# Performance work log

Measured on AMD Instinct MI355X. Metric: run time of the kernel, lower is better.

The kernel has to match this reference:

```python
import jax, jax.numpy as jnp
import numpy as np

B, IN_DIM, HV_DIM, NUM_CLASSES = 16384, 2048, 8192, 1000


def setup_inputs() -> dict:
    key = jax.random.key(0)
    kx, kp, kc = jax.random.split(key, 3)
    x = jax.random.normal(kx, (B, IN_DIM), dtype=jnp.float32)
    # +/-1 random projection and class hypervectors (2*bernoulli - 1), as in the torch buffers
    proj = (jax.random.randint(kp, (IN_DIM, HV_DIM), 0, 2) * 2 - 1).astype(jnp.float32)
    class_hv = (jax.random.randint(kc, (HV_DIM, NUM_CLASSES), 0, 2) * 2 - 1).astype(jnp.float32)
    return {"x": x, "proj": proj, "class_hv": class_hv}


def reference(x, proj, class_hv):
    # dense projection -> sign binarize -> binary associative-memory matmul (score_mode='dot')
    hv = x @ proj                                   # [B, HV_DIM]
    hv_bin = jnp.where(hv >= 0, 1.0, -1.0).astype(hv.dtype)
    scores = hv_bin @ class_hv                      # [B, NUM_CLASSES]
    return scores, hv_bin
```

## Files before the change

### kernel.cpp

```cpp
#include <hip/hip_runtime.h>
#include <hip/hip_bf16.h>

typedef _Float16 half8  __attribute__((ext_vector_type(8)));
typedef _Float16 half4_t __attribute__((ext_vector_type(4)));
typedef float    floatx4 __attribute__((ext_vector_type(4)));
typedef int      intx4   __attribute__((ext_vector_type(4)));

#define B_DIM   16384
#define IN_D    2048
#define HV_D    8192
#define NC      1000
#define NCP     1024
#define SCORES_N (B_DIM * NC)

#define GLD16(gp, lp) __builtin_amdgcn_global_load_lds( \
    (const __attribute__((address_space(1))) void*)(gp), \
    (__attribute__((address_space(3))) void*)(lp), 16, 0, 0)

__global__ void k_split(const float* __restrict__ x, _Float16* __restrict__ xh,
                        _Float16* __restrict__ xl) {
    size_t i = (size_t)blockIdx.x * 256 + threadIdx.x;
    floatx4 v = ((const floatx4*)x)[i];
    half4_t h, l;
#pragma unroll
    for (int j = 0; j < 4; ++j) {
        _Float16 hh = (_Float16)v[j];
        h[j] = hh;
        l[j] = (_Float16)(v[j] - (float)hh);
    }
    ((half4_t*)xh)[i] = h;
    ((half4_t*)xl)[i] = l;
}

__global__ void k_transpose_proj(const float* __restrict__ p, _Float16* __restrict__ pT) {
    __shared__ float tile[64][65];
    const int t = threadIdx.x;
    const int nt = blockIdx.x * 64;
    const int kt = blockIdx.y * 64;
    const int tr = t >> 4, tc = (t & 15) * 4;
#pragma unroll
    for (int s = 0; s < 4; ++s) {
        int r = tr + s * 16;
        floatx4 v = *(const floatx4*)&p[(size_t)(kt + r) * HV_D + nt + tc];
        tile[r][tc] = v[0]; tile[r][tc + 1] = v[1];
        tile[r][tc + 2] = v[2]; tile[r][tc + 3] = v[3];
    }
    __syncthreads();
#pragma unroll
    for (int s = 0; s < 4; ++s) {
        int rn = tr + s * 16;
        half4_t o;
#pragma unroll
        for (int j = 0; j < 4; ++j) o[j] = (_Float16)tile[tc + j][rn];
        *(half4_t*)&pT[(size_t)(nt + rn) * IN_D + kt + tc] = o;
    }
}

__global__ void k_pack_class(const float* __restrict__ c, signed char* __restrict__ cT) {
    int tid = blockIdx.x * 256 + threadIdx.x;
    int idx = tid * 4;
    int n = idx >> 13;
    int k = idx & (HV_D - 1);
    int w = 0;
    if (n < NC) {
#pragma unroll
        for (int j = 0; j < 4; ++j) {
            float v = c[(size_t)(k + j) * NC + n];
            int b = (v >= 0.f) ? 1 : -1;
            w |= (b & 0xff) << (8 * j);
        }
    }
    *(int*)&cT[(size_t)n * HV_D + k] = w;
}

__launch_bounds__(256, 2)
__global__ void k_gemm1(const _Float16* __restrict__ xh, const _Float16* __restrict__ xl,
                        const _Float16* __restrict__ pT,
                        float* __restrict__ hv_out, signed char* __restrict__ hvb) {
    __shared__ _Float16 sAh[128 * 64];
    __shared__ _Float16 sAl[128 * 64];
    __shared__ _Float16 sB [256 * 64];
    const int t = threadIdx.x;
    const int w = t >> 6, l = t & 63;
    const int m0 = blockIdx.y * 128, n0 = blockIdx.x * 256;
    const int wm = (w >> 1) * 64, wn = (w & 1) * 128;
    const int lm = l & 15, kq = l >> 4;
    const int srow  = w * 8 + (l >> 3);
    const int scol  = (((l & 7) ^ ((l >> 3) & 7))) * 8;
    const int sbyte = w * 1024 + l * 16;

    floatx4 acc[4][8] = {};

    for (int k0 = 0; k0 < IN_D; k0 += 64) {
        __syncthreads();
#pragma unroll
        for (int i = 0; i < 4; ++i) {
            const size_t ga = (size_t)(m0 + srow + i * 32) * IN_D + k0 + scol;
            const int lo = sbyte + i * 4096;
            GLD16(xh + ga, (char*)sAh + lo);
            GLD16(xl + ga, (char*)sAl + lo);
        }
#pragma unroll
        for (int i = 0; i < 8; ++i) {
            const size_t gb = (size_t)(n0 + srow + i * 32) * IN_D + k0 + scol;
            GLD16(pT + gb, (char*)sB + sbyte + i * 4096);
        }
        __syncthreads();
#pragma unroll
        for (int ks = 0; ks < 2; ++ks) {
            const int csw = ((ks * 4 + kq) ^ (lm & 7)) * 8;
            half8 b[8];
#pragma unroll
            for (int ns = 0; ns < 8; ++ns)
                b[ns] = *(const half8*)&sB[(wn + ns * 16 + lm) * 64 + csw];
#pragma unroll
            for (int ms = 0; ms < 4; ++ms) {
                half8 a = *(const half8*)&sAh[(wm + ms * 16 + lm) * 64 + csw];
#pragma unroll
                for (int ns = 0; ns < 8; ++ns)
                    acc[ms][ns] = __builtin_amdgcn_mfma_f32_16x16x32_f16(a, b[ns], acc[ms][ns], 0, 0, 0);
            }
#pragma unroll
            for (int ms = 0; ms < 4; ++ms) {
                half8 a = *(const half8*)&sAl[(wm + ms * 16 + lm) * 64 + csw];
#pragma unroll
                for (int ns = 0; ns < 8; ++ns)
                    acc[ms][ns] = __builtin_amdgcn_mfma_f32_16x16x32_f16(a, b[ns], acc[ms][ns], 0, 0, 0);
            }
        }
    }

#pragma unroll
    for (int ms = 0; ms < 4; ++ms) {
#pragma unroll
        for (int ns = 0; ns < 8; ++ns) {
            const int m = m0 + wm + ms * 16 + kq * 4;
            const int n = n0 + wn + ns * 16 + lm;
#pragma unroll
            for (int r = 0; r < 4; ++r) {
                const int pos = (acc[ms][ns][r] >= 0.f);
                const size_t o = (size_t)(m + r) * HV_D + n;
                hv_out[o] = pos ? 1.f : -1.f;
                hvb[o] = (signed char)(pos ? 1 : -1);
            }
        }
    }
}

__launch_bounds__(256, 2)
__global__ void k_gemm2(const signed char* __restrict__ hvb, const signed char* __restrict__ cT,
                        float* __restrict__ scores) {
    __shared__ signed char sA[128 * 128];
    __shared__ signed char sB[256 * 128];
    const int t = threadIdx.x;
    const int w = t >> 6, l = t & 63;
    const int m0 = blockIdx.y * 128, n0 = blockIdx.x * 256;
    const int wm = (w >> 1) * 64, wn = (w & 1) * 128;
    const int lm = l & 15, kq = l >> 4;
    const int srow  = w * 8 + (l >> 3);
    const int scol  = (((l & 7) ^ ((l >> 3) & 7))) * 16;
    const int sbyte = w * 1024 + l * 16;

    intx4 acc[4][8] = {};

    for (int k0 = 0; k0 < HV_D; k0 += 128) {
        __syncthreads();
#pragma unroll
        for (int i = 0; i < 4; ++i)
            GLD16(hvb + (size_t)(m0 + srow + i * 32) * HV_D + k0 + scol,
                  (char*)sA + sbyte + i * 4096);
#pragma unroll
        for (int i = 0; i < 8; ++i)
            GLD16(cT + (size_t)(n0 + srow + i * 32) * HV_D + k0 + scol,
                  (char*)sB + sbyte + i * 4096);
        __syncthreads();
#pragma unroll
        for (int ks = 0; ks < 2; ++ks) {
            const int csw = ((ks * 4 + kq) ^ (lm & 7)) * 16;
            intx4 b[8];
#pragma unroll
            for (int ns = 0; ns < 8; ++ns)
                b[ns] = *(const intx4*)&sB[(wn + ns * 16 + lm) * 128 + csw];
#pragma unroll
            for (int ms = 0; ms < 4; ++ms) {
                intx4 a = *(const intx4*)&sA[(wm + ms * 16 + lm) * 128 + csw];
#pragma unroll
                for (int ns = 0; ns < 8; ++ns)
                    acc[ms][ns] = __builtin_amdgcn_mfma_i32_16x16x64_i8(a, b[ns], acc[ms][ns], 0, 0, 0);
            }
        }
    }

#pragma unroll
    for (int ms = 0; ms < 4; ++ms) {
#pragma unroll
        for (int ns = 0; ns < 8; ++ns) {
            const int m = m0 + wm + ms * 16 + kq * 4;
            const int n = n0 + wn + ns * 16 + lm;
            if (n < NC) {
#pragma unroll
                for (int r = 0; r < 4; ++r)
                    scores[(size_t)(m + r) * NC + n] = (float)acc[ms][ns][r];
            }
        }
    }
}

extern "C" void kernel_launch(void* const* d_in, const int* in_sizes, int n_in,
                              void* d_out, int out_size, void* d_ws, size_t ws_size,
                              hipStream_t stream) {
    const float* x    = (const float*)d_in[0];
    const float* proj = (const float*)d_in[1];
    const float* chv  = (const float*)d_in[2];
    float* out    = (float*)d_out;
    float* scores = out;
    float* hv_out = out + (size_t)SCORES_N;

    char* ws = (char*)d_ws;
    _Float16*    xh  = (_Float16*)(ws);
    _Float16*    xl  = (_Float16*)(ws + (size_t)67108864);
    _Float16*    pT  = (_Float16*)(ws + (size_t)134217728);
    signed char* cT  = (signed char*)(ws + (size_t)167772160);
    signed char* hvb = (signed char*)(ws + (size_t)176160768);

    k_split<<<(B_DIM * IN_D / 4) / 256, 256, 0, stream>>>(x, xh, xl);
    k_transpose_proj<<<dim3(HV_D / 64, IN_D / 64), 256, 0, stream>>>(proj, pT);
    k_pack_class<<<(NCP * HV_D / 4) / 256, 256, 0, stream>>>(chv, cT);
    k_gemm1<<<dim3(HV_D / 256, B_DIM / 128), 256, 0, stream>>>(xh, xl, pT, hv_out, hvb);
    k_gemm2<<<dim3(NCP / 256, B_DIM / 128), 256, 0, stream>>>(hvb, cT, scores);
}
```

Measured before the change: 1.630 ms.

## Double-buffer LDS in both GEMMs and tile-transpose class packing

Both GEMM kernels switch from single-buffered LDS with two barriers per K step to a double-buffered ping-pong. The next K slice is loaded asynchronously with global_load_lds while the current one feeds MFMA, and the K step is halved to keep LDS size the same. The XOR swizzle is reworked for the narrower 32-half / 64-byte rows. Separately, the class-vector packing kernel now uses a shared-memory tile transpose so global reads are coalesced. This adds more iterations and barriers per K, and the narrower swizzle risks more LDS bank conflicts.

```diff
diff --git a/kernel.cpp b/kernel.cpp
--- a/kernel.cpp
+++ b/kernel.cpp
@@ -57,76 +57,87 @@
 }
 
 __global__ void k_pack_class(const float* __restrict__ c, signed char* __restrict__ cT) {
-    int tid = blockIdx.x * 256 + threadIdx.x;
-    int idx = tid * 4;
-    int n = idx >> 13;
-    int k = idx & (HV_D - 1);
-    int w = 0;
-    if (n < NC) {
-#pragma unroll
-        for (int j = 0; j < 4; ++j) {
-            float v = c[(size_t)(k + j) * NC + n];
-            int b = (v >= 0.f) ? 1 : -1;
-            w |= (b & 0xff) << (8 * j);
-        }
-    }
-    *(int*)&cT[(size_t)n * HV_D + k] = w;
+    __shared__ signed char tile[64][68];
+    const int t = threadIdx.x;
+    const int nt = blockIdx.x * 64;
+    const int kt = blockIdx.y * 64;
+    const int nl = t & 63;
+    const int n = nt + nl;
+#pragma unroll
+    for (int s = 0; s < 16; ++s) {
+        const int kl = s * 4 + (t >> 6);
+        signed char v = 0;
+        if (n < NC) {
+            float f = c[(size_t)(kt + kl) * NC + n];
+            v = (f >= 0.f) ? (signed char)1 : (signed char)-1;
+        }
+        tile[kl][nl] = v;
+    }
+    __syncthreads();
+    const int wn = t >> 2;
+    const int wk = (t & 3) * 16;
+    intx4 o;
+    signed char* ob = (signed char*)&o;
+#pragma unroll
+    for (int j = 0; j < 16; ++j) ob[j] = tile[wk + j][wn];
+    *(intx4*)&cT[(size_t)(nt + wn) * HV_D + kt + wk] = o;
 }
 
 __launch_bounds__(256, 2)
 __global__ void k_gemm1(const _Float16* __restrict__ xh, const _Float16* __restrict__ xl,
                         const _Float16* __restrict__ pT,
                         float* __restrict__ hv_out, signed char* __restrict__ hvb) {
-    __shared__ _Float16 sAh[128 * 64];
-    __shared__ _Float16 sAl[128 * 64];
-    __shared__ _Float16 sB [256 * 64];
+    __shared__ _Float16 sAh[2][128 * 32];
+    __shared__ _Float16 sAl[2][128 * 32];
+    __shared__ _Float16 sB [2][256 * 32];
     const int t = threadIdx.x;
     const int w = t >> 6, l = t & 63;
     const int m0 = blockIdx.y * 128, n0 = blockIdx.x * 256;
     const int wm = (w >> 1) * 64, wn = (w & 1) * 128;
     const int lm = l & 15, kq = l >> 4;
-    const int srow  = w * 8 + (l >> 3);
-    const int scol  = (((l & 7) ^ ((l >> 3) & 7))) * 8;
-    const int sbyte = w * 1024 + l * 16;
+    const int sr  = t >> 2;
+    const int sch = (t & 3) ^ ((sr ^ (sr >> 2)) & 3);
+    const int csw = ((kq ^ ((lm ^ (lm >> 2)) & 3)) & 3) * 8;
 
     floatx4 acc[4][8] = {};
 
-    for (int k0 = 0; k0 < IN_D; k0 += 64) {
+    auto stage = [&](int k0, int p) {
+#pragma unroll
+        for (int i = 0; i < 2; ++i) {
+            const size_t ga = (size_t)(m0 + i * 64 + sr) * IN_D + k0 + sch * 8;
+            GLD16(xh + ga, (char*)&sAh[p][i * 2048] + t * 16);
+            GLD16(xl + ga, (char*)&sAl[p][i * 2048] + t * 16);
+        }
+#pragma unroll
+        for (int i = 0; i < 4; ++i) {
+            const size_t gb = (size_t)(n0 + i * 64 + sr) * IN_D + k0 + sch * 8;
+            GLD16(pT + gb, (char*)&sB[p][i * 2048] + t * 16);
+        }
+    };
+
+    stage(0, 0);
+    const int NIT = IN_D / 32;
+    for (int it = 0; it < NIT; ++it) {
+        const int p = it & 1;
         __syncthreads();
-#pragma unroll
-        for (int i = 0; i < 4; ++i) {
-            const size_t ga = (size_t)(m0 + srow + i * 32) * IN_D + k0 + scol;
-            const int lo = sbyte + i * 4096;
-            GLD16(xh + ga, (char*)sAh + lo);
-            GLD16(xl + ga, (char*)sAl + lo);
-        }
-#pragma unroll
-        for (int i = 0; i < 8; ++i) {
-            const size_t gb = (size_t)(n0 + srow + i * 32) * IN_D + k0 + scol;
-            GLD16(pT + gb, (char*)sB + sbyte + i * 4096);
-        }
-        __syncthreads();
-#pragma unroll
-        for (int ks = 0; ks < 2; ++ks) {
-            const int csw = ((ks * 4 + kq) ^ (lm & 7)) * 8;
-            half8 b[8];
+        if (it + 1 < NIT) stage((it + 1) * 32, p ^ 1);
+        half8 b[8];
+#pragma unroll
+        for (int ns = 0; ns < 8; ++ns)
+            b[ns] = *(const half8*)&sB[p][(wn + ns * 16 + lm) * 32 + csw];
+#pragma unroll
+        for (int ms = 0; ms < 4; ++ms) {
+            half8 a = *(const half8*)&sAh[p][(wm + ms * 16 + lm) * 32 + csw];
 #pragma unroll
             for (int ns = 0; ns < 8; ++ns)
-                b[ns] = *(const half8*)&sB[(wn + ns * 16 + lm) * 64 + csw];
-#pragma unroll
-            for (int ms = 0; ms < 4; ++ms) {
-                half8 a = *(const half8*)&sAh[(wm + ms * 16 + lm) * 64 + csw];
-#pragma unroll
-                for (int ns = 0; ns < 8; ++ns)
-                    acc[ms][ns] = __builtin_amdgcn_mfma_f32_16x16x32_f16(a, b[ns], acc[ms][ns], 0, 0, 0);
-            }
-#pragma unroll
-            for (int ms = 0; ms < 4; ++ms) {
-                half8 a = *(const half8*)&sAl[(wm + ms * 16 + lm) * 64 + csw];
-#pragma unroll
-                for (int ns = 0; ns < 8; ++ns)
-                    acc[ms][ns] = __builtin_amdgcn_mfma_f32_16x16x32_f16(a, b[ns], acc[ms][ns], 0, 0, 0);
-            }
+                acc[ms][ns] = __builtin_amdgcn_mfma_f32_16x16x32_f16(a, b[ns], acc[ms][ns], 0, 0, 0);
+        }
+#pragma unroll
+        for (int ms = 0; ms < 4; ++ms) {
+            half8 a = *(const half8*)&sAl[p][(wm + ms * 16 + lm) * 32 + csw];
+#pragma unroll
+            for (int ns = 0; ns < 8; ++ns)
+                acc[ms][ns] = __builtin_amdgcn_mfma_f32_16x16x32_f16(a, b[ns], acc[ms][ns], 0, 0, 0);
         }
     }
 
@@ -150,44 +161,46 @@
 __launch_bounds__(256, 2)
 __global__ void k_gemm2(const signed char* __restrict__ hvb, const signed char* __restrict__ cT,
                         float* __restrict__ scores) {
-    __shared__ signed char sA[128 * 128];
-    __shared__ signed char sB[256 * 128];
+    __shared__ signed char sA[2][128 * 64];
+    __shared__ signed char sB[2][256 * 64];
     const int t = threadIdx.x;
     const int w = t >> 6, l = t & 63;
     const int m0 = blockIdx.y * 128, n0 = blockIdx.x * 256;
     const int wm = (w >> 1) * 64, wn = (w & 1) * 128;
     const int lm = l & 15, kq = l >> 4;
-    const int srow  = w * 8 + (l >> 3);
-    const int scol  = (((l & 7) ^ ((l >> 3) & 7))) * 16;
-    const int sbyte = w * 1024 + l * 16;
+    const int sr  = t >> 2;
+    const int sch = (t & 3) ^ ((sr ^ (sr >> 2)) & 3);
+    const int csw = ((kq ^ ((lm ^ (lm >> 2)) & 3)) & 3) * 16;
 
     intx4 acc[4][8] = {};
 
-    for (int k0 = 0; k0 < HV_D; k0 += 128) {
+    auto stage = [&](int k0, int p) {
+#pragma unroll
+        for (int i = 0; i < 2; ++i)
+            GLD16(hvb + (size_t)(m0 + i * 64 + sr) * HV_D + k0 + sch * 16,
+                  (char*)&sA[p][i * 4096] + t * 16);
+#pragma unroll
+        for (int i = 0; i < 4; ++i)
+            GLD16(cT + (size_t)(n0 + i * 64 + sr) * HV_D + k0 + sch * 16,
+                  (char*)&sB[p][i * 4096] + t * 16);
+    };
+
+    stage(0, 0);
+    const int NIT = HV_D / 64;
+    for (int it = 0; it < NIT; ++it) {
+        const int p = it & 1;
         __syncthreads();
-#pragma unroll
-        for (int i = 0; i < 4; ++i)
-            GLD16(hvb + (size_t)(m0 + srow + i * 32) * HV_D + k0 + scol,
-                  (char*)sA + sbyte + i * 4096);
-#pragma unroll
-        for (int i = 0; i < 8; ++i)
-            GLD16(cT + (size_t)(n0 + srow + i * 32) * HV_D + k0 + scol,
-                  (char*)sB + sbyte + i * 4096);
-        __syncthreads();
-#pragma unroll
-        for (int ks = 0; ks < 2; ++ks) {
-            const int csw = ((ks * 4 + kq) ^ (lm & 7)) * 16;
-            intx4 b[8];
+        if (it + 1 < NIT) stage((it + 1) * 64, p ^ 1);
+        intx4 b[8];
+#pragma unroll
+        for (int ns = 0; ns < 8; ++ns)
+            b[ns] = *(const intx4*)&sB[p][(wn + ns * 16 + lm) * 64 + csw];
+#pragma unroll
+        for (int ms = 0; ms < 4; ++ms) {
+            intx4 a = *(const intx4*)&sA[p][(wm + ms * 16 + lm) * 64 + csw];
 #pragma unroll
             for (int ns = 0; ns < 8; ++ns)
-                b[ns] = *(const intx4*)&sB[(wn + ns * 16 + lm) * 128 + csw];
-#pragma unroll
-            for (int ms = 0; ms < 4; ++ms) {
-                intx4 a = *(const intx4*)&sA[(wm + ms * 16 + lm) * 128 + csw];
-#pragma unroll
-                for (int ns = 0; ns < 8; ++ns)
-                    acc[ms][ns] = __builtin_amdgcn_mfma_i32_16x16x64_i8(a, b[ns], acc[ms][ns], 0, 0, 0);
-            }
+                acc[ms][ns] = __builtin_amdgcn_mfma_i32_16x16x64_i8(a, b[ns], acc[ms][ns], 0, 0, 0);
         }
     }
 
@@ -225,7 +238,7 @@
 
     k_split<<<(B_DIM * IN_D / 4) / 256, 256, 0, stream>>>(x, xh, xl);
     k_transpose_proj<<<dim3(HV_D / 64, IN_D / 64), 256, 0, stream>>>(proj, pT);
-    k_pack_class<<<(NCP * HV_D / 4) / 256, 256, 0, stream>>>(chv, cT);
+    k_pack_class<<<dim3(NCP / 64, HV_D / 64), 256, 0, stream>>>(chv, cT);
     k_gemm1<<<dim3(HV_D / 256, B_DIM / 128), 256, 0, stream>>>(xh, xl, pT, hv_out, hvb);
     k_gemm2<<<dim3(NCP / 256, B_DIM / 128), 256, 0, stream>>>(hvb, cT, scores);
 }
```

Measured after the change: 1.794 ms. +10.1%, slower.
